# Optimization experiments

Measured on AMD Instinct MI355X. Metric: run time of the kernel, lower is better.

Reference implementation:

```python
import jax, jax.numpy as jnp
jax.config.update("jax_enable_x64", True)
import numpy as np

B, S, D, H = 2, 1024, 1024, 16
DEPTH = D // H  # 64


def setup_inputs() -> dict:
    key = jax.random.key(0)
    ks = jax.random.split(key, 12)
    inp = {
        "q": jax.random.normal(ks[0], (B, S, D), jnp.float32),
        "k": jax.random.normal(ks[1], (B, S, D), jnp.float32),
        "v": jax.random.normal(ks[2], (B, S - 1, D), jnp.float32),
        "e": jnp.zeros((1,), jnp.float32),  # unused by the layer
        "mask": jax.random.randint(ks[3], (B, S - 1, S - 1), 0, 2, jnp.int32),
        "Wq": jax.random.normal(ks[4], (D, D), jnp.float32) * 0.02,
        "bq": jnp.zeros((D,), jnp.float32),
        "Wk": jax.random.normal(ks[5], (D, D), jnp.float32) * 0.02,
        "bk": jnp.zeros((D,), jnp.float32),
        "Wv": jax.random.normal(ks[6], (D, D), jnp.float32) * 0.02,
        "bv": jnp.zeros((D,), jnp.float32),
        "Wo": jax.random.normal(ks[7], (D, D), jnp.float32) * 0.02,
        "bo": jnp.zeros((D,), jnp.float32),
    }
    return inp


def _split_heads(x, b):
    # [b, s, D] -> [b, H, s, DEPTH]
    return x.reshape(b, -1, H, DEPTH).transpose(0, 2, 1, 3)


def reference(q, k, v, e, mask, Wq, bq, Wk, bk, Wv, bv, Wo, bo):
    b = q.shape[0]
    qh = _split_heads(q @ Wq + bq, b)  # [b,H,S,dh]
    kh = _split_heads(k @ Wk + bk, b)  # [b,H,S,dh]
    vh = _split_heads(v @ Wv + bv, b)  # [b,H,S-1,dh]
    # QK^T then asymmetric offset slice [1:, :-1]
    scores = jnp.einsum("bhqd,bhkd->bhqk", qh, kh)[:, :, 1:, :-1]  # [b,H,S-1,S-1]
    inv_sqrt_dk = 1.0 / jnp.sqrt(jnp.float32(DEPTH))
    nl_qk = jax.nn.relu(scores * inv_sqrt_dk).astype(jnp.float64)
    nl_qk = nl_qk + mask[:, None, :, :].astype(jnp.float64) * (-1e9)
    att_weights = jax.nn.softmax(nl_qk, axis=-1)  # fp64, [b,H,S-1,S-1]
    out = jnp.einsum("bhqk,bhkd->bhqd", att_weights, vh.astype(jnp.float64))
    out = out.transpose(0, 2, 1, 3).reshape(b, -1, H * DEPTH)  # [b,S-1,D]
    output = out.astype(jnp.float32) @ Wo + bo
    return (output, att_weights)
```

## Files before the change

### kernel.cpp

```cpp
#include <hip/hip_runtime.h>
#include <math.h>

#define HN 16
#define SEQ 1024
#define DMODEL 1024
#define DH 64
#define SM1 1023

typedef float  f32x4  __attribute__((ext_vector_type(4)));
typedef __bf16 bf16x8 __attribute__((ext_vector_type(8)));

#define GLD16(gsrc, ldst) \
    __builtin_amdgcn_global_load_lds((const __attribute__((address_space(1))) void*)(gsrc), \
                                     (__attribute__((address_space(3))) void*)(ldst), 16, 0, 0)

__global__ __launch_bounds__(256)
void split3_kernel(const float* __restrict__ s0, __bf16* __restrict__ h0, __bf16* __restrict__ l0, int n0,
                   const float* __restrict__ s1, __bf16* __restrict__ h1, __bf16* __restrict__ l1, int n1,
                   const float* __restrict__ s2, __bf16* __restrict__ h2, __bf16* __restrict__ l2, int n2)
{
    const float* src; __bf16* hi; __bf16* lo; int nchunks;
    if (blockIdx.y == 0)      { src = s0; hi = h0; lo = l0; nchunks = n0; }
    else if (blockIdx.y == 1) { src = s1; hi = h1; lo = l1; nchunks = n1; }
    else                      { src = s2; hi = h2; lo = l2; nchunks = n2; }

    for (int i = blockIdx.x * 256 + threadIdx.x; i < nchunks; i += gridDim.x * 256) {
        float4 v0 = *(const float4*)&src[(size_t)i * 8];
        float4 v1 = *(const float4*)&src[(size_t)i * 8 + 4];
        float xa[8] = {v0.x, v0.y, v0.z, v0.w, v1.x, v1.y, v1.z, v1.w};
        bf16x8 h8, l8;
#pragma unroll
        for (int e = 0; e < 8; ++e) {
            __bf16 hb = (__bf16)xa[e];
            h8[e] = hb;
            l8[e] = (__bf16)(xa[e] - (float)hb);
        }
        *(bf16x8*)&hi[(size_t)i * 8] = h8;
        *(bf16x8*)&lo[(size_t)i * 8] = l8;
    }
}

__global__ __launch_bounds__(256)
void splitT4_kernel(const float* __restrict__ W0, __bf16* __restrict__ th0, __bf16* __restrict__ tl0,
                    const float* __restrict__ W1, __bf16* __restrict__ th1, __bf16* __restrict__ tl1,
                    const float* __restrict__ W2, __bf16* __restrict__ th2, __bf16* __restrict__ tl2,
                    const float* __restrict__ W3, __bf16* __restrict__ th3, __bf16* __restrict__ tl3)
{
    const float* W; __bf16* thi; __bf16* tlo;
    const int z = blockIdx.z;
    if (z == 0)      { W = W0; thi = th0; tlo = tl0; }
    else if (z == 1) { W = W1; thi = th1; tlo = tl1; }
    else if (z == 2) { W = W2; thi = th2; tlo = tl2; }
    else             { W = W3; thi = th3; tlo = tl3; }

    __shared__ float T[64][65];
    const int t = threadIdx.x;
    const int r0 = blockIdx.y * 64, c0 = blockIdx.x * 64;
#pragma unroll
    for (int it = 0; it < 4; ++it) {
        const int rl = (t >> 4) + it * 16;
        const int cl = (t & 15) * 4;
        float4 v = *(const float4*)&W[(size_t)(r0 + rl) * 1024 + c0 + cl];
        T[cl + 0][rl] = v.x; T[cl + 1][rl] = v.y;
        T[cl + 2][rl] = v.z; T[cl + 3][rl] = v.w;
    }
    __syncthreads();
    const int nl = t >> 2, ch = t & 3;
    float vals[16];
#pragma unroll
    for (int e = 0; e < 16; ++e) vals[e] = T[nl][ch * 16 + e];
    bf16x8 h0, h1, l0, l1;
#pragma unroll
    for (int e = 0; e < 8; ++e) {
        __bf16 hb = (__bf16)vals[e];
        h0[e] = hb; l0[e] = (__bf16)(vals[e] - (float)hb);
        __bf16 hb2 = (__bf16)vals[8 + e];
        h1[e] = hb2; l1[e] = (__bf16)(vals[8 + e] - (float)hb2);
    }
    const size_t base = (size_t)(c0 + nl) * 1024 + r0 + ch * 16;
    *(bf16x8*)&thi[base] = h0; *(bf16x8*)&thi[base + 8] = h1;
    *(bf16x8*)&tlo[base] = l0; *(bf16x8*)&tlo[base + 8] = l1;
}

template<int MODE>
__global__ __launch_bounds__(256)
void gemm_bf16_kernel(const __bf16* __restrict__ Ahi, const __bf16* __restrict__ Alo,
                      const __bf16* __restrict__ Bhi, const __bf16* __restrict__ Blo,
                      const float* __restrict__ bias, float* __restrict__ out32,
                      __bf16* __restrict__ outHi, __bf16* __restrict__ outLo,
                      int M, int rows)
{
    __shared__ __align__(16) char LB[32768];

    const int t = threadIdx.x, w = t >> 6, l = t & 63;
    const int lr = l & 15, ls = l >> 4;
    const int m0 = blockIdx.y * 64, n0 = blockIdx.x * 64;

    f32x4 acc[4];
#pragma unroll
    for (int ct = 0; ct < 4; ++ct) acc[ct] = f32x4{0.f, 0.f, 0.f, 0.f};

    const int ar   = w * 16 + lr;
    const int a_hi = ar * 128 + (((2 * ls    ) ^ (ar & 7)) << 4);
    const int a_lo = ar * 128 + (((2 * ls + 1) ^ (ar & 7)) << 4);

    const __bf16* aA[2];
    const __bf16* bB[2];
#pragma unroll
    for (int i = 0; i < 2; ++i) {
        const int r = (w * 2 + i) * 8 + (l >> 3);
        const int un = (l & 7) ^ (r & 7);
        aA[i] = ((un & 1) ? Alo : Ahi) + (size_t)(m0 + r) * 1024 + (un >> 1) * 8;
        bB[i] = ((un & 1) ? Blo : Bhi) + (size_t)(n0 + r) * 1024 + (un >> 1) * 8;
    }

#define GSTAGE(k0_, buf_) {                                                       \
    _Pragma("unroll")                                                             \
    for (int i_ = 0; i_ < 2; ++i_) {                                              \
        GLD16(aA[i_] + (k0_), LB + (buf_) * 8192 + (w * 2 + i_) * 1024);          \
        GLD16(bB[i_] + (k0_), LB + 16384 + (buf_) * 8192 + (w * 2 + i_) * 1024);  \
    } }

    GSTAGE(0, 0);
    __syncthreads();

    for (int ks = 0; ks < 32; ++ks) {
        const int cur = ks & 1;
        if (ks < 31) GSTAGE((ks + 1) * 32, cur ^ 1);

        const char* As = LB + cur * 8192;
        const char* Bs = LB + 16384 + cur * 8192;
        const bf16x8 ah = *(const bf16x8*)(As + a_hi);
        const bf16x8 al = *(const bf16x8*)(As + a_lo);
        __builtin_amdgcn_s_setprio(1);
#pragma unroll
        for (int ct = 0; ct < 4; ++ct) {
            const int bc   = ct * 16 + lr;
            const int b_hi = bc * 128 + (((2 * ls    ) ^ (bc & 7)) << 4);
            const int b_lo = bc * 128 + (((2 * ls + 1) ^ (bc & 7)) << 4);
            const bf16x8 bh = *(const bf16x8*)(Bs + b_hi);
            const bf16x8 bl = *(const bf16x8*)(Bs + b_lo);
            acc[ct] = __builtin_amdgcn_mfma_f32_16x16x32_bf16(ah, bh, acc[ct], 0, 0, 0);
            acc[ct] = __builtin_amdgcn_mfma_f32_16x16x32_bf16(al, bh, acc[ct], 0, 0, 0);
            acc[ct] = __builtin_amdgcn_mfma_f32_16x16x32_bf16(ah, bl, acc[ct], 0, 0, 0);
        }
        __builtin_amdgcn_s_setprio(0);
        __syncthreads();
    }
#undef GSTAGE

    if (MODE == 2) {
        float* T = (float*)LB;
#pragma unroll
        for (int ct = 0; ct < 4; ++ct) {
            const int nl = ct * 16 + lr;
            const float bv = bias[n0 + nl];
#pragma unroll
            for (int j = 0; j < 4; ++j)
                T[nl * 65 + w * 16 + ls * 4 + j] = acc[ct][j] + bv;
        }
        __syncthreads();
        const int dr = t >> 2, ch = t & 3;
        const int hh = n0 >> 6;
        const int mb = m0 + ch * 16;
        float vals[16];
#pragma unroll
        for (int e = 0; e < 16; ++e) vals[e] = T[dr * 65 + ch * 16 + e];
        const int bb0 = mb / rows;
        const int s0  = mb - bb0 * rows;
        if (mb + 15 < M && bb0 == (mb + 15) / rows && (s0 & 7) == 0) {
            bf16x8 h0, h1, l0, l1;
#pragma unroll
            for (int e = 0; e < 8; ++e) {
                __bf16 hb = (__bf16)vals[e];
                h0[e] = hb; l0[e] = (__bf16)(vals[e] - (float)hb);
                __bf16 hb2 = (__bf16)vals[8 + e];
                h1[e] = hb2; l1[e] = (__bf16)(vals[8 + e] - (float)hb2);
            }
            const size_t base = (((size_t)(bb0 * HN + hh) * DH + dr) << 10) + s0;
            *(bf16x8*)&outHi[base] = h0; *(bf16x8*)&outHi[base + 8] = h1;
            *(bf16x8*)&outLo[base] = l0; *(bf16x8*)&outLo[base + 8] = l1;
        } else {
#pragma unroll
            for (int e = 0; e < 16; ++e) {
                const int m = mb + e;
                if (m < M) {
                    const int bb = m / rows, s = m - bb * rows;
                    const size_t idx = (((size_t)(bb * HN + hh) * DH + dr) << 10) + s;
                    const __bf16 hb = (__bf16)vals[e];
                    outHi[idx] = hb;
                    outLo[idx] = (__bf16)(vals[e] - (float)hb);
                }
            }
        }
    } else {
#pragma unroll
        for (int ct = 0; ct < 4; ++ct) {
            const int n = n0 + ct * 16 + lr;
            const float bv = bias[n];
#pragma unroll
            for (int j = 0; j < 4; ++j) {
                const int m = m0 + w * 16 + ls * 4 + j;
                if (m >= M) continue;
                const float val = acc[ct][j] + bv;
                if (MODE == 1) {
                    out32[(size_t)m * DMODEL + n] = val;
                } else {
                    const int bb = m / rows, s = m - bb * rows;
                    const __bf16 hb = (__bf16)val;
                    const __bf16 lb = (__bf16)(val - (float)hb);
                    const size_t idx = (((size_t)(bb * HN + (n >> 6)) * SEQ + s) << 6) + (n & 63);
                    outHi[idx] = hb; outLo[idx] = lb;
                }
            }
        }
    }
}

__global__ __launch_bounds__(256)
void mask_pack_kernel(const int* __restrict__ mask, unsigned int* __restrict__ mb)
{
    const int row = blockIdx.x * 4 + (threadIdx.x >> 6);
    const int l   = threadIdx.x & 63;
    if (row >= 2 * SM1) return;
    const int* mrow = mask + (size_t)row * SM1;
    unsigned int* out = mb + (size_t)row * 32;
#pragma unroll
    for (int i = 0; i < 16; ++i) {
        const int c = i * 64 + l;
        const bool mv = (c < SM1) && (mrow[c] != 0);
        unsigned long long bal = __ballot(mv);
        if (l == 0) {
            out[i * 2]     = (unsigned int)bal;
            out[i * 2 + 1] = (unsigned int)(bal >> 32);
        }
    }
}

__global__ __launch_bounds__(512, 4)
void attn_fused_kernel(const __bf16* __restrict__ qhi, const __bf16* __restrict__ qlo,
                       const __bf16* __restrict__ khi, const __bf16* __restrict__ klo,
                       const __bf16* __restrict__ vthi, const __bf16* __restrict__ vtlo,
                       const unsigned int* __restrict__ mbG,
                       float* __restrict__ att,
                       __bf16* __restrict__ ctxHi, __bf16* __restrict__ ctxLo)
{
    __shared__ __align__(16) char QE[17408];
    __shared__ __align__(16) char Kb[2][16384];
    __shared__ __align__(16) char Vb[16384];
    __shared__ unsigned int mbitsT[32][64];
    __shared__ float invs[64];
    __shared__ float partial[64][2];

    const int id  = blockIdx.x;
    const int xcd = id & 7, slot = id >> 3;
    const int bh  = xcd + 8 * (slot >> 4);
    const int b   = bh >> 4, h = bh & 15;
    const int q0  = (slot & 15) * 64;

    const int t = threadIdx.x, w = t >> 6, l = t & 63;
    const int lr = l & 15, ls = l >> 4;
    const int g = w & 3, p = w >> 2;

    const __bf16* kA[2];
    const __bf16* vA[2];
#pragma unroll
    for (int i = 0; i < 2; ++i) {
        const int seg = w * 2 + i;
        const int r  = seg * 4 + (l >> 4);
        const int cw = (l & 15) ^ (r & 15);
        kA[i] = ((cw >> 3) ? klo : khi) + ((size_t)bh * SEQ + r) * DH + (cw & 7) * 8;
        vA[i] = ((cw >> 3) ? vtlo : vthi) + (((size_t)bh * DH + r) << 10) + (cw & 7) * 8;
    }

#define KDMA(koff_, b_) {                                                       \
    _Pragma("unroll")                                                           \
    for (int i_ = 0; i_ < 2; ++i_)                                              \
        GLD16(kA[i_] + (koff_), Kb[b_] + (w * 2 + i_) * 1024);                  \
    }
#define VDMA(coff_) {                                                           \
    _Pragma("unroll")                                                           \
    for (int i_ = 0; i_ < 2; ++i_)                                              \
        GLD16(vA[i_] + (coff_), Vb + (w * 2 + i_) * 1024);                      \
    }

#pragma unroll
    for (int i = 0; i < 2; ++i) {
        const int seg = w * 2 + i;
        const int r = seg * 4 + (l >> 4);
        const int cw = (l & 15) ^ (r & 15);
        int qrow = q0 + r + 1; if (qrow > 1023) qrow = 1023;
        const __bf16* src = ((cw >> 3) ? qlo : qhi)
            + ((size_t)bh * SEQ + qrow) * DH + (cw & 7) * 8;
        GLD16(src, QE + seg * 1024);
    }
    KDMA(0, 0);
#pragma unroll
    for (int it = 0; it < 4; ++it) {
        const int idm = t + it * 512;
        const int cw = idm & 31, r = idm >> 5;
        const int rr = q0 + r;
        mbitsT[cw][r] = (rr < SM1) ? mbG[((size_t)b * SM1 + rr) * 32 + cw] : 0u;
    }
    __syncthreads();

    const int arow = g * 16 + lr;
    const bf16x8 a0h = *(const bf16x8*)(QE + arow * 256 + (((ls     ) ^ lr) << 4));
    const bf16x8 a1h = *(const bf16x8*)(QE + arow * 256 + ((( 4 + ls) ^ lr) << 4));
    const bf16x8 a0l = *(const bf16x8*)(QE + arow * 256 + ((( 8 + ls) ^ lr) << 4));
    const bf16x8 a1l = *(const bf16x8*)(QE + arow * 256 + (((12 + ls) ^ lr) << 4));
    __syncthreads();

    float rsum[4] = {0.f, 0.f, 0.f, 0.f};
    for (int kt = 0; kt < 16; ++kt) {
        const char* KB = Kb[kt & 1];
        if (kt < 15) KDMA((kt + 1) * 4096, (kt + 1) & 1);

#pragma unroll
        for (int i = 0; i < 2; ++i) {
            const int ct = p * 2 + i;
            const int kr16 = ct * 16 + lr;
            const bf16x8 b0h = *(const bf16x8*)(KB + kr16 * 256 + (((ls     ) ^ lr) << 4));
            const bf16x8 b1h = *(const bf16x8*)(KB + kr16 * 256 + ((( 4 + ls) ^ lr) << 4));
            const bf16x8 b0l = *(const bf16x8*)(KB + kr16 * 256 + ((( 8 + ls) ^ lr) << 4));
            const bf16x8 b1l = *(const bf16x8*)(KB + kr16 * 256 + (((12 + ls) ^ lr) << 4));

            f32x4 acc = {0.f, 0.f, 0.f, 0.f};
            __builtin_amdgcn_s_setprio(1);
            acc = __builtin_amdgcn_mfma_f32_16x16x32_bf16(a0h, b0h, acc, 0, 0, 0);
            acc = __builtin_amdgcn_mfma_f32_16x16x32_bf16(a0l, b0h, acc, 0, 0, 0);
            acc = __builtin_amdgcn_mfma_f32_16x16x32_bf16(a0h, b0l, acc, 0, 0, 0);
            acc = __builtin_amdgcn_mfma_f32_16x16x32_bf16(a1h, b1h, acc, 0, 0, 0);
            acc = __builtin_amdgcn_mfma_f32_16x16x32_bf16(a1l, b1h, acc, 0, 0, 0);
            acc = __builtin_amdgcn_mfma_f32_16x16x32_bf16(a1h, b1l, acc, 0, 0, 0);
            __builtin_amdgcn_s_setprio(0);

            const int c = kt * 64 + ct * 16 + lr;
            const int wmi = kt * 2 + (ct >> 1);
#pragma unroll
            for (int j = 0; j < 4; ++j) {
                const int r = q0 + g * 16 + ls * 4 + j;
                if (r < SM1 && c < SM1) {
                    float sc = fmaxf(acc[j] * 0.125f, 0.f);
                    const unsigned int wm = mbitsT[wmi][g * 16 + ls * 4 + j];
                    if ((wm >> ((ct & 1) * 16 + lr)) & 1u) sc = -1e9f;
                    rsum[j] += __expf(sc);
                }
            }
        }
        __syncthreads();
    }

    KDMA(0, 0);

#pragma unroll
    for (int j = 0; j < 4; ++j) {
        rsum[j] += __shfl_xor(rsum[j], 1, 64);
        rsum[j] += __shfl_xor(rsum[j], 2, 64);
        rsum[j] += __shfl_xor(rsum[j], 4, 64);
        rsum[j] += __shfl_xor(rsum[j], 8, 64);
    }
    if (lr == 0) {
#pragma unroll
        for (int j = 0; j < 4; ++j)
            partial[g * 16 + ls * 4 + j][p] = rsum[j];
    }
    __syncthreads();
    if (t < 64) {
        const float s = partial[t][0] + partial[t][1];
        invs[t] = (q0 + t < SM1) ? 1.0f / s : 0.f;
    }
    __syncthreads();
    float inv4[4];
#pragma unroll
    for (int j = 0; j < 4; ++j) inv4[j] = invs[g * 16 + ls * 4 + j];

    float* E = (float*)QE;
    f32x4 oacc[4];
#pragma unroll
    for (int ct = 0; ct < 4; ++ct) oacc[ct] = f32x4{0.f, 0.f, 0.f, 0.f};

    for (int kt = 0; kt < 16; ++kt) {
        const int c0 = kt * 64;
        const char* KB = Kb[kt & 1];
        VDMA(c0);
        if (kt < 15) KDMA((kt + 1) * 4096, (kt + 1) & 1);

#pragma unroll
        for (int i = 0; i < 2; ++i) {
            const int ct = p * 2 + i;
            const int kr16 = ct * 16 + lr;
            const bf16x8 b0h = *(const bf16x8*)(KB + kr16 * 256 + (((ls     ) ^ lr) << 4));
            const bf16x8 b1h = *(const bf16x8*)(KB + kr16 * 256 + ((( 4 + ls) ^ lr) << 4));
            const bf16x8 b0l = *(const bf16x8*)(KB + kr16 * 256 + ((( 8 + ls) ^ lr) << 4));
            const bf16x8 b1l = *(const bf16x8*)(KB + kr16 * 256 + (((12 + ls) ^ lr) << 4));

            f32x4 acc = {0.f, 0.f, 0.f, 0.f};
            __builtin_amdgcn_s_setprio(1);
            acc = __builtin_amdgcn_mfma_f32_16x16x32_bf16(a0h, b0h, acc, 0, 0, 0);
            acc = __builtin_amdgcn_mfma_f32_16x16x32_bf16(a0l, b0h, acc, 0, 0, 0);
            acc = __builtin_amdgcn_mfma_f32_16x16x32_bf16(a0h, b0l, acc, 0, 0, 0);
            acc = __builtin_amdgcn_mfma_f32_16x16x32_bf16(a1h, b1h, acc, 0, 0, 0);
            acc = __builtin_amdgcn_mfma_f32_16x16x32_bf16(a1l, b1h, acc, 0, 0, 0);
            acc = __builtin_amdgcn_mfma_f32_16x16x32_bf16(a1h, b1l, acc, 0, 0, 0);
            __builtin_amdgcn_s_setprio(0);

            const int c = c0 + ct * 16 + lr;
            const int wmi = kt * 2 + (ct >> 1);
#pragma unroll
            for (int j = 0; j < 4; ++j) {
                const int r = q0 + g * 16 + ls * 4 + j;
                float v = 0.f;
                if (r < SM1 && c < SM1) {
                    float sc = fmaxf(acc[j] * 0.125f, 0.f);
                    const unsigned int wm = mbitsT[wmi][g * 16 + ls * 4 + j];
                    if ((wm >> ((ct & 1) * 16 + lr)) & 1u) sc = -1e9f;
                    v = __expf(sc) * inv4[j];
                }
                E[(g * 16 + ls * 4 + j) * 68 + ct * 16 + lr] = v;
            }
        }
        __syncthreads();

#pragma unroll
        for (int it = 0; it < 2; ++it) {
            const int idw = t + it * 512;
            const int r = idw >> 4, q4 = idw & 15;
            const int rr = q0 + r, cc = c0 + q4 * 4;
            if (rr < SM1) {
                f32x4 vv = *(const f32x4*)&E[r * 68 + q4 * 4];
                float* dst = &att[((size_t)bh * SM1 + rr) * SM1 + cc];
                if (cc + 4 <= SM1) {
                    __builtin_nontemporal_store(vv, (f32x4*)dst);
                } else {
                    if (cc + 0 < SM1) dst[0] = vv.x;
                    if (cc + 1 < SM1) dst[1] = vv.y;
                    if (cc + 2 < SM1) dst[2] = vv.z;
                }
            }
        }

        {
            const int pr = g * 16 + lr;
            const f32x4 p0 = *(const f32x4*)&E[pr * 68 + p * 32 + ls * 8];
            const f32x4 p1 = *(const f32x4*)&E[pr * 68 + p * 32 + ls * 8 + 4];
            float pf[8] = {p0.x, p0.y, p0.z, p0.w, p1.x, p1.y, p1.z, p1.w};
            bf16x8 ph, pl;
#pragma unroll
            for (int e = 0; e < 8; ++e) {
                const __bf16 hb = (__bf16)pf[e];
                ph[e] = hb;
                pl[e] = (__bf16)(pf[e] - (float)hb);
            }
#pragma unroll
            for (int ct = 0; ct < 4; ++ct) {
                const int vr16 = ct * 16 + lr;
                const bf16x8 vh = *(const bf16x8*)(Vb + vr16 * 256 + (((p * 4 + ls    ) ^ lr) << 4));
                const bf16x8 vl = *(const bf16x8*)(Vb + vr16 * 256 + (((8 + p * 4 + ls) ^ lr) << 4));
                __builtin_amdgcn_s_setprio(1);
                oacc[ct] = __builtin_amdgcn_mfma_f32_16x16x32_bf16(ph, vh, oacc[ct], 0, 0, 0);
                oacc[ct] = __builtin_amdgcn_mfma_f32_16x16x32_bf16(pl, vh, oacc[ct], 0, 0, 0);
                oacc[ct] = __builtin_amdgcn_mfma_f32_16x16x32_bf16(ph, vl, oacc[ct], 0, 0, 0);
                __builtin_amdgcn_s_setprio(0);
            }
        }
        __syncthreads();
    }

    float* red = (float*)QE;
    if (p == 1) {
#pragma unroll
        for (int ct = 0; ct < 4; ++ct)
#pragma unroll
            for (int j = 0; j < 4; ++j)
                red[(g * 16 + ls * 4 + j) * 68 + ct * 16 + lr] = oacc[ct][j];
    }
    __syncthreads();
    if (p == 0) {
#pragma unroll
        for (int ct = 0; ct < 4; ++ct)
#pragma unroll
            for (int j = 0; j < 4; ++j) {
                const int r = q0 + g * 16 + ls * 4 + j;
                if (r < SM1) {
                    const float val =
                        oacc[ct][j] + red[(g * 16 + ls * 4 + j) * 68 + ct * 16 + lr];
                    const size_t idx =
                        ((size_t)b * SM1 + r) * DMODEL + h * DH + ct * 16 + lr;
                    const __bf16 hb = (__bf16)val;
                    ctxHi[idx] = hb;
                    ctxLo[idx] = (__bf16)(val - (float)hb);
                }
            }
    }
#undef KDMA
#undef VDMA
}

extern "C" void kernel_launch(void* const* d_in, const int* in_sizes, int n_in,
                              void* d_out, int out_size, void* d_ws, size_t ws_size,
                              hipStream_t stream) {
    const float* q    = (const float*)d_in[0];
    const float* k    = (const float*)d_in[1];
    const float* v    = (const float*)d_in[2];
    const int*   mask = (const int*)  d_in[4];
    const float* Wq   = (const float*)d_in[5];
    const float* bq   = (const float*)d_in[6];
    const float* Wk   = (const float*)d_in[7];
    const float* bk   = (const float*)d_in[8];
    const float* Wv   = (const float*)d_in[9];
    const float* bv   = (const float*)d_in[10];
    const float* Wo   = (const float*)d_in[11];
    const float* bo   = (const float*)d_in[12];

    float* out0 = (float*)d_out;
    float* att  = out0 + (size_t)2 * SM1 * DMODEL;

    const size_t NX  = (size_t)2048 * 1024;
    const size_t NW  = (size_t)1024 * 1024;
    const size_t NQH = (size_t)2 * HN * SEQ * DH;
    const size_t NVT = (size_t)2 * HN * DH * 1024;

    __bf16* p2  = (__bf16*)d_ws;
    __bf16* qSh = p2; p2 += NX;  __bf16* qSl = p2; p2 += NX;
    __bf16* kSh = p2; p2 += NX;  __bf16* kSl = p2; p2 += NX;
    __bf16* vSh = p2; p2 += NX;  __bf16* vSl = p2; p2 += NX;
    __bf16* WqTh = p2; p2 += NW; __bf16* WqTl = p2; p2 += NW;
    __bf16* WkTh = p2; p2 += NW; __bf16* WkTl = p2; p2 += NW;
    __bf16* WvTh = p2; p2 += NW; __bf16* WvTl = p2; p2 += NW;
    __bf16* WoTh = p2; p2 += NW; __bf16* WoTl = p2; p2 += NW;
    __bf16* qhh = p2; p2 += NQH; __bf16* qhl = p2; p2 += NQH;
    __bf16* khh = p2; p2 += NQH; __bf16* khl = p2; p2 += NQH;
    __bf16* vth = p2; p2 += NVT; __bf16* vtl = p2; p2 += NVT;
    unsigned int* mbG = (unsigned int*)p2;
    __bf16* ctxHi = qSh;
    __bf16* ctxLo = qSl;

    (void)hipMemsetAsync(vth, 0, 2 * NVT * sizeof(__bf16), stream);

    mask_pack_kernel<<<dim3(512), 256, 0, stream>>>(mask, mbG);

    split3_kernel<<<dim3(512, 3), 256, 0, stream>>>(
        q, qSh, qSl, 2048 * 1024 / 8,
        k, kSh, kSl, 2048 * 1024 / 8,
        v, vSh, vSl, 2046 * 1024 / 8);

    splitT4_kernel<<<dim3(16, 16, 4), 256, 0, stream>>>(
        Wq, WqTh, WqTl, Wk, WkTh, WkTl, Wv, WvTh, WvTl, Wo, WoTh, WoTl);

    gemm_bf16_kernel<0><<<dim3(16, 32), 256, 0, stream>>>(qSh, qSl, WqTh, WqTl, bq,
                                                          nullptr, qhh, qhl, 2 * SEQ, SEQ);
    gemm_bf16_kernel<0><<<dim3(16, 32), 256, 0, stream>>>(kSh, kSl, WkTh, WkTl, bk,
                                                          nullptr, khh, khl, 2 * SEQ, SEQ);
    gemm_bf16_kernel<2><<<dim3(16, 32), 256, 0, stream>>>(vSh, vSl, WvTh, WvTl, bv,
                                                          nullptr, vth, vtl, 2 * SM1, SM1);

    attn_fused_kernel<<<dim3(512), 512, 0, stream>>>(qhh, qhl, khh, khl, vth, vtl,
                                                     mbG, att, ctxHi, ctxLo);

    gemm_bf16_kernel<1><<<dim3(16, 32), 256, 0, stream>>>(ctxHi, ctxLo, WoTh, WoTl, bo,
                                                          out0, nullptr, nullptr, 2 * SM1, SM1);
}
```

Baseline: 227.9 us.

## Shrink LDS footprint to raise occupancy; read mask bits from global

Drops the second K double-buffer and the shared mask-bit tile so the fused attention kernel needs less LDS, and raises the launch-bounds occupancy hint from 4 to 6 blocks. In the row-sum pass the V buffer stands in as the second K buffer. In the output pass the K and V loads for the next tile are issued right after the barriers that free their buffers. Mask words are now loaded per thread straight from global memory each tile. The trade-off is less prefetch overlap in the second pass, more scattered global mask loads, and tighter register limits from the higher occupancy target.

Result: slower. 323.7 us (+42.1%).

```diff
diff --git a/kernel.cpp b/kernel.cpp
--- a/kernel.cpp
+++ b/kernel.cpp
@@ -237,7 +237,7 @@
     }
 }
 
-__global__ __launch_bounds__(512, 4)
+__global__ __launch_bounds__(512, 6)
 void attn_fused_kernel(const __bf16* __restrict__ qhi, const __bf16* __restrict__ qlo,
                        const __bf16* __restrict__ khi, const __bf16* __restrict__ klo,
                        const __bf16* __restrict__ vthi, const __bf16* __restrict__ vtlo,
@@ -246,9 +246,8 @@
                        __bf16* __restrict__ ctxHi, __bf16* __restrict__ ctxLo)
 {
     __shared__ __align__(16) char QE[17408];
-    __shared__ __align__(16) char Kb[2][16384];
+    __shared__ __align__(16) char Kb[16384];
     __shared__ __align__(16) char Vb[16384];
-    __shared__ unsigned int mbitsT[32][64];
     __shared__ float invs[64];
     __shared__ float partial[64][2];
 
@@ -272,11 +271,18 @@
         kA[i] = ((cw >> 3) ? klo : khi) + ((size_t)bh * SEQ + r) * DH + (cw & 7) * 8;
         vA[i] = ((cw >> 3) ? vtlo : vthi) + (((size_t)bh * DH + r) << 10) + (cw & 7) * 8;
     }
-
-#define KDMA(koff_, b_) {                                                       \
+    const unsigned int* mrow4[4];
+#pragma unroll
+    for (int j = 0; j < 4; ++j) {
+        int r = q0 + g * 16 + ls * 4 + j;
+        if (r > SM1 - 1) r = SM1 - 1;
+        mrow4[j] = mbG + ((size_t)b * SM1 + r) * 32 + p;
+    }
+
+#define KDMA(koff_, dst_) {                                                     \
     _Pragma("unroll")                                                           \
     for (int i_ = 0; i_ < 2; ++i_)                                              \
-        GLD16(kA[i_] + (koff_), Kb[b_] + (w * 2 + i_) * 1024);                  \
+        GLD16(kA[i_] + (koff_), (dst_) + (w * 2 + i_) * 1024);                  \
     }
 #define VDMA(coff_) {                                                           \
     _Pragma("unroll")                                                           \
@@ -294,14 +300,7 @@
             + ((size_t)bh * SEQ + qrow) * DH + (cw & 7) * 8;
         GLD16(src, QE + seg * 1024);
     }
-    KDMA(0, 0);
-#pragma unroll
-    for (int it = 0; it < 4; ++it) {
-        const int idm = t + it * 512;
-        const int cw = idm & 31, r = idm >> 5;
-        const int rr = q0 + r;
-        mbitsT[cw][r] = (rr < SM1) ? mbG[((size_t)b * SM1 + rr) * 32 + cw] : 0u;
-    }
+    KDMA(0, Kb);
     __syncthreads();
 
     const int arow = g * 16 + lr;
@@ -313,8 +312,12 @@
 
     float rsum[4] = {0.f, 0.f, 0.f, 0.f};
     for (int kt = 0; kt < 16; ++kt) {
-        const char* KB = Kb[kt & 1];
-        if (kt < 15) KDMA((kt + 1) * 4096, (kt + 1) & 1);
+        const char* KB = (kt & 1) ? Vb : Kb;
+        if (kt < 15) KDMA((kt + 1) * 4096, (kt & 1) ? Kb : Vb);
+
+        unsigned int wm4[4];
+#pragma unroll
+        for (int j = 0; j < 4; ++j) wm4[j] = mrow4[j][kt * 2];
 
 #pragma unroll
         for (int i = 0; i < 2; ++i) {
@@ -336,14 +339,12 @@
             __builtin_amdgcn_s_setprio(0);
 
             const int c = kt * 64 + ct * 16 + lr;
-            const int wmi = kt * 2 + (ct >> 1);
 #pragma unroll
             for (int j = 0; j < 4; ++j) {
                 const int r = q0 + g * 16 + ls * 4 + j;
                 if (r < SM1 && c < SM1) {
                     float sc = fmaxf(acc[j] * 0.125f, 0.f);
-                    const unsigned int wm = mbitsT[wmi][g * 16 + ls * 4 + j];
-                    if ((wm >> ((ct & 1) * 16 + lr)) & 1u) sc = -1e9f;
+                    if ((wm4[j] >> ((ct & 1) * 16 + lr)) & 1u) sc = -1e9f;
                     rsum[j] += __expf(sc);
                 }
             }
@@ -351,7 +352,8 @@
         __syncthreads();
     }
 
-    KDMA(0, 0);
+    KDMA(0, Kb);
+    VDMA(0);
 
 #pragma unroll
     for (int j = 0; j < 4; ++j) {
@@ -382,18 +384,19 @@
 
     for (int kt = 0; kt < 16; ++kt) {
         const int c0 = kt * 64;
-        const char* KB = Kb[kt & 1];
-        VDMA(c0);
-        if (kt < 15) KDMA((kt + 1) * 4096, (kt + 1) & 1);
+
+        unsigned int wm4[4];
+#pragma unroll
+        for (int j = 0; j < 4; ++j) wm4[j] = mrow4[j][kt * 2];
 
 #pragma unroll
         for (int i = 0; i < 2; ++i) {
             const int ct = p * 2 + i;
             const int kr16 = ct * 16 + lr;
-            const bf16x8 b0h = *(const bf16x8*)(KB + kr16 * 256 + (((ls     ) ^ lr) << 4));
-            const bf16x8 b1h = *(const bf16x8*)(KB + kr16 * 256 + ((( 4 + ls) ^ lr) << 4));
-            const bf16x8 b0l = *(const bf16x8*)(KB + kr16 * 256 + ((( 8 + ls) ^ lr) << 4));
-            const bf16x8 b1l = *(const bf16x8*)(KB + kr16 * 256 + (((12 + ls) ^ lr) << 4));
+            const bf16x8 b0h = *(const bf16x8*)(Kb + kr16 * 256 + (((ls     ) ^ lr) << 4));
+            const bf16x8 b1h = *(const bf16x8*)(Kb + kr16 * 256 + ((( 4 + ls) ^ lr) << 4));
+            const bf16x8 b0l = *(const bf16x8*)(Kb + kr16 * 256 + ((( 8 + ls) ^ lr) << 4));
+            const bf16x8 b1l = *(const bf16x8*)(Kb + kr16 * 256 + (((12 + ls) ^ lr) << 4));
 
             f32x4 acc = {0.f, 0.f, 0.f, 0.f};
             __builtin_amdgcn_s_setprio(1);
@@ -406,21 +409,21 @@
             __builtin_amdgcn_s_setprio(0);
 
             const int c = c0 + ct * 16 + lr;
-            const int wmi = kt * 2 + (ct >> 1);
 #pragma unroll
             for (int j = 0; j < 4; ++j) {
                 const int r = q0 + g * 16 + ls * 4 + j;
                 float v = 0.f;
                 if (r < SM1 && c < SM1) {
                     float sc = fmaxf(acc[j] * 0.125f, 0.f);
-                    const unsigned int wm = mbitsT[wmi][g * 16 + ls * 4 + j];
-                    if ((wm >> ((ct & 1) * 16 + lr)) & 1u) sc = -1e9f;
+                    if ((wm4[j] >> ((ct & 1) * 16 + lr)) & 1u) sc = -1e9f;
                     v = __expf(sc) * inv4[j];
                 }
                 E[(g * 16 + ls * 4 + j) * 68 + ct * 16 + lr] = v;
             }
         }
         __syncthreads();
+
+        if (kt < 15) KDMA((kt + 1) * 4096, Kb);
 
 #pragma unroll
         for (int it = 0; it < 2; ++it) {
@@ -465,6 +468,8 @@
             }
         }
         __syncthreads();
+
+        if (kt < 15) VDMA((kt + 1) * 64);
     }
 
     float* red = (float*)QE;
```
